# Kernel optimization log

Measured on AMD Instinct MI355X. Metric: run time of the kernel, lower is better.

## Reference

```python
import jax, jax.numpy as jnp
import numpy as np

NUM_KNOTS = 10
DEGREE = 3
NUM_BASIS = NUM_KNOTS + DEGREE - 1  # 12
IN_FEATURES = 512
OUT_FEATURES = 512


def _interval_bounds():
    # t = linspace(0,1,num_knots); segment i covers [t[max(0,i-deg+1)], t[min(i+1,K-1)])
    t = np.linspace(0.0, 1.0, NUM_KNOTS, dtype=np.float32)
    idx = np.arange(NUM_BASIS)
    lower = t[np.maximum(0, idx - (DEGREE - 1))]
    upper = t[np.minimum(idx + 1, NUM_KNOTS - 1)]
    return jnp.asarray(lower), jnp.asarray(upper)


def setup_inputs() -> dict:
    key = jax.random.key(0)
    kx, kc = jax.random.split(key)
    x = jax.random.uniform(kx, (8, 2048, IN_FEATURES), dtype=jnp.float32)
    # coeffs for spline (i=out, j=in): torch indexes splines[i*in_features+j]
    coeffs = jax.random.normal(kc, (OUT_FEATURES, IN_FEATURES, NUM_BASIS), dtype=jnp.float32)
    return {"x": x, "coeffs": coeffs}


def reference(x, coeffs):
    lower, upper = _interval_bounds()  # [NUM_BASIS] each
    # piecewise-constant basis masks: [b, s, in, NUM_BASIS]
    xe = x[..., None]
    basis = ((xe >= lower) & (xe < upper)).astype(x.dtype)
    # out[b,s,i] = sum_j sum_k basis[b,s,j,k] * coeffs[i,j,k]
    return jnp.einsum("bsjk,ijk->bsi", basis, coeffs)
```

## Files before the change

kernel.cpp:

```cpp
#include <hip/hip_runtime.h>

#define MTOT 16384
#define NFEAT 512
#define KTOT 4608

typedef float f32x4 __attribute__((ext_vector_type(4)));
typedef short s16x8 __attribute__((ext_vector_type(8)));

__device__ __forceinline__ int div9(int c) { return (c * 7282) >> 16; }

#define GLDS(GP, LP) __builtin_amdgcn_global_load_lds( \
    (const __attribute__((address_space(1))) void*)(GP), \
    (__attribute__((address_space(3))) void*)(LP), 16, 0, 0)

__device__ __forceinline__ s16x8 decode_mask(unsigned msk) {
  unsigned e0 = (msk & 15u) * 0x00204081u & 0x01010101u;
  unsigned e1 = (msk >> 4)  * 0x00204081u & 0x01010101u;
  unsigned d0 = __builtin_amdgcn_perm(e0, e0, 0x0C010C00u) * 0x3F80u;
  unsigned d1 = __builtin_amdgcn_perm(e0, e0, 0x0C030C02u) * 0x3F80u;
  unsigned d2 = __builtin_amdgcn_perm(e1, e1, 0x0C010C00u) * 0x3F80u;
  unsigned d3 = __builtin_amdgcn_perm(e1, e1, 0x0C030C02u) * 0x3F80u;
  union { unsigned d[4]; s16x8 v; } u;
  u.d[0] = d0; u.d[1] = d1; u.d[2] = d2; u.d[3] = d3;
  return u.v;
}

__global__ __launch_bounds__(256) void prep(const float* __restrict__ x,
                                            const float* __restrict__ coeffs,
                                            unsigned char* __restrict__ codeT,
                                            unsigned short* __restrict__ Bmat) {
  __shared__ unsigned char segt[64][68];
  const int bx = blockIdx.x;
  const int tid = threadIdx.x;
  if (bx < 2048) {
    const int i = bx >> 2, q = bx & 3;
    const float* cb = coeffs + (size_t)i * 6144;
#pragma unroll
    for (int p = 0; p < 5; ++p) {
      int kl = p * 256 + tid;
      if (kl < 1152) {
        int k = q * 1152 + kl;
        int j = div9(k), s = k - j * 9;
        float v = cb[j * 12 + s] + cb[j * 12 + s + 1] + cb[j * 12 + s + 2];
        unsigned u = __float_as_uint(v);
        unsigned rn = (u + 0x7FFFu + ((u >> 16) & 1u)) >> 16;
        Bmat[(size_t)i * KTOT + k] = (unsigned short)rn;
      }
    }
  } else {
    const int bb = bx - 2048;
    const int mt = bb >> 3;
    const int jt = bb & 7;
    const int m0 = mt * 64;
    const float4* x4 = (const float4*)x;
    const float T1 = (float)(1.0/9.0), T2 = (float)(2.0/9.0), T3 = (float)(3.0/9.0),
                T4 = (float)(4.0/9.0), T5 = (float)(5.0/9.0), T6 = (float)(6.0/9.0),
                T7 = (float)(7.0/9.0), T8 = (float)(8.0/9.0);
#pragma unroll
    for (int it = 0; it < 4; ++it) {
      int f = it * 256 + tid;
      int m = f >> 4, jq = f & 15;
      float4 v = x4[(size_t)(m0 + m) * 128 + jt * 16 + jq];
      uchar4 sv;
      { float xv = v.x; sv.x = (unsigned char)((xv>=T1)+(xv>=T2)+(xv>=T3)+(xv>=T4)+(xv>=T5)+(xv>=T6)+(xv>=T7)+(xv>=T8)); }
      { float xv = v.y; sv.y = (unsigned char)((xv>=T1)+(xv>=T2)+(xv>=T3)+(xv>=T4)+(xv>=T5)+(xv>=T6)+(xv>=T7)+(xv>=T8)); }
      { float xv = v.z; sv.z = (unsigned char)((xv>=T1)+(xv>=T2)+(xv>=T3)+(xv>=T4)+(xv>=T5)+(xv>=T6)+(xv>=T7)+(xv>=T8)); }
      { float xv = v.w; sv.w = (unsigned char)((xv>=T1)+(xv>=T2)+(xv>=T3)+(xv>=T4)+(xv>=T5)+(xv>=T6)+(xv>=T7)+(xv>=T8)); }
      *(uchar4*)&segt[m][jq * 4] = sv;
    }
    __syncthreads();
#pragma unroll
    for (int p = 0; p < 5; ++p) {
      int u = p * 256 + tid;
      if (u < 1152) {
        int gl = u >> 4, mq = u & 15;
        int c0 = jt * 576 + gl * 8;
        int j0 = div9(c0), j1 = div9(c0 + 7);
        int j0l = j0 - jt * 64, j1l = j1 - jt * 64;
        uchar4 ob;
        unsigned char* pb = (unsigned char*)&ob;
#pragma unroll
        for (int c = 0; c < 4; ++c) {
          int m = mq * 4 + c;
          int s0 = segt[m][j0l];
          int pos0 = j0 * 9 + s0 - c0;
          unsigned code = (pos0 >= 0 && pos0 < 8) ? (1u << pos0) : 0u;
          if (j1 != j0) {
            int s1 = segt[m][j1l];
            int pos1 = j1 * 9 + s1 - c0;
            if (pos1 < 8) code |= (1u << pos1);
          }
          pb[c] = (unsigned char)code;
        }
        *(uchar4*)(codeT + (size_t)(jt * 72 + gl) * MTOT + m0 + mq * 4) = ob;
      }
    }
  }
}

__global__ __launch_bounds__(256, 4) void kan_gemm(const unsigned char* __restrict__ codeT,
                                                   const unsigned short* __restrict__ Bmat,
                                                   float* __restrict__ out) {
  __shared__ __align__(16) short Blds[2][8 * 512];
  const int tid = threadIdx.x;
  const int lane = tid & 63;
  const int wid = tid >> 6;
  const int lm = lane & 15;
  const int lq = lane >> 4;
  const int bx = blockIdx.x;
  const int nt = bx & 7;
  const int mt = bx >> 3;
  const int m0 = mt * 128, n0 = nt * 64;

  const unsigned short* gB = Bmat + (size_t)(n0 + wid * 16 + lm) * KTOT + lq * 8;
  const unsigned char* gC0 = codeT + (size_t)lq * MTOT + m0 + wid * 32 + lm;
  const unsigned char* gC1 = codeT + (size_t)(4 + lq) * MTOT + m0 + wid * 32 + lm;

  f32x4 acc[2][4] = {};
  s16x8 afA[4], afB[4];
  unsigned char cr[4];

#define LOAD_CR() do { \
    cr[0] = gC0[0]; cr[1] = gC1[0]; cr[2] = gC0[16]; cr[3] = gC1[16]; \
    gC0 += (size_t)8 * MTOT; gC1 += (size_t)8 * MTOT; } while (0)

#define ISSUE_B(buf) do { \
    short* base = &Blds[buf][0] + wid * 1024; \
    GLDS(gB,      base);        \
    GLDS(gB + 32, base + 512);  \
    gB += 64; } while (0)

#define COMPUTE(AF, buf) do { \
    _Pragma("unroll") \
    for (int ks = 0; ks < 2; ++ks) { \
      s16x8 bf[4]; \
      _Pragma("unroll") \
      for (int ns = 0; ns < 4; ++ns) \
        bf[ns] = *(const s16x8*)&Blds[buf][(ns * 2 + ks) * 512 + lane * 8]; \
      _Pragma("unroll") \
      for (int ms = 0; ms < 2; ++ms) \
        _Pragma("unroll") \
        for (int ns = 0; ns < 4; ++ns) \
          acc[ms][ns] = __builtin_amdgcn_mfma_f32_16x16x32_bf16(AF[ms * 2 + ks], bf[ns], acc[ms][ns], 0, 0, 0); \
    } } while (0)

  LOAD_CR();
  ISSUE_B(0);
#pragma unroll
  for (int f = 0; f < 4; ++f) afA[f] = decode_mask(cr[f]);
  LOAD_CR();
  __syncthreads();

#pragma unroll 1
  for (int kt = 0; kt < 72; kt += 2) {
    ISSUE_B(1);
#pragma unroll
    for (int f = 0; f < 4; ++f) afB[f] = decode_mask(cr[f]);
    if (kt < 70) LOAD_CR();
    COMPUTE(afA, 0);
    __syncthreads();
    if (kt < 70) {
      ISSUE_B(0);
#pragma unroll
      for (int f = 0; f < 4; ++f) afA[f] = decode_mask(cr[f]);
      LOAD_CR();
    }
    COMPUTE(afB, 1);
    __syncthreads();
  }

#pragma unroll
  for (int ms = 0; ms < 2; ++ms) {
#pragma unroll
    for (int ns = 0; ns < 4; ++ns) {
      int tok = m0 + wid * 32 + ms * 16 + lq * 4;
      int col = n0 + ns * 16 + lm;
      float* op = out + (size_t)tok * NFEAT + col;
#pragma unroll
      for (int rg = 0; rg < 4; ++rg) op[(size_t)rg * NFEAT] = acc[ms][ns][rg];
    }
  }
}

extern "C" void kernel_launch(void* const* d_in, const int* in_sizes, int n_in,
                              void* d_out, int out_size, void* d_ws, size_t ws_size,
                              hipStream_t stream) {
  const float* x = (const float*)d_in[0];
  const float* coeffs = (const float*)d_in[1];
  float* out = (float*)d_out;
  unsigned char* codeT = (unsigned char*)d_ws;
  unsigned short* Bmat = (unsigned short*)((char*)d_ws + (size_t)576 * MTOT);

  prep<<<dim3(4096), dim3(256), 0, stream>>>(x, coeffs, codeT, Bmat);
  kan_gemm<<<dim3(1024), dim3(256), 0, stream>>>(codeT, Bmat, out);
}
```

Measured before the change: 173.3 us.

## Switch GEMM to 32x32x16 MFMA with 256-row tiles and inline mask decode

Replaces the 16x16x32 bf16 MFMA tiling with 32x32x16 MFMA, doubling the M tile per block to 256 rows and halving the grid to 512 blocks. Each wave now computes a 64x64 output tile, so each B fragment loaded from LDS is reused across more rows, and the LDS layout and global-to-LDS loads are reorganised to match. Mask decoding moves inside the compute loop instead of being precomputed one stage ahead. Occupancy hint drops from 4 to 2 blocks per CU, with larger accumulators per thread. With only 512 blocks, CU utilisation may suffer on a 256-CU part.

```diff
diff --git a/kernel.cpp b/kernel.cpp
--- a/kernel.cpp
+++ b/kernel.cpp
@@ -4,7 +4,7 @@
 #define NFEAT 512
 #define KTOT 4608
 
-typedef float f32x4 __attribute__((ext_vector_type(4)));
+typedef float f32x16 __attribute__((ext_vector_type(16)));
 typedef short s16x8 __attribute__((ext_vector_type(8)));
 
 __device__ __forceinline__ int div9(int c) { return (c * 7282) >> 16; }
@@ -98,86 +98,86 @@
   }
 }
 
-__global__ __launch_bounds__(256, 4) void kan_gemm(const unsigned char* __restrict__ codeT,
+__global__ __launch_bounds__(256, 2) void kan_gemm(const unsigned char* __restrict__ codeT,
                                                    const unsigned short* __restrict__ Bmat,
                                                    float* __restrict__ out) {
   __shared__ __align__(16) short Blds[2][8 * 512];
   const int tid = threadIdx.x;
   const int lane = tid & 63;
   const int wid = tid >> 6;
-  const int lm = lane & 15;
-  const int lq = lane >> 4;
+  const int l5 = lane & 31;
+  const int lh = lane >> 5;
   const int bx = blockIdx.x;
   const int nt = bx & 7;
   const int mt = bx >> 3;
-  const int m0 = mt * 128, n0 = nt * 64;
+  const int m0 = mt * 256, n0 = nt * 64;
 
-  const unsigned short* gB = Bmat + (size_t)(n0 + wid * 16 + lm) * KTOT + lq * 8;
-  const unsigned char* gC0 = codeT + (size_t)lq * MTOT + m0 + wid * 32 + lm;
-  const unsigned char* gC1 = codeT + (size_t)(4 + lq) * MTOT + m0 + wid * 32 + lm;
+  const int s0 = 2 * wid, s1 = 2 * wid + 1;
+  const unsigned short* gB0 = Bmat + (size_t)(n0 + (s0 >> 2) * 32 + l5) * KTOT + (s0 & 3) * 16 + lh * 8;
+  const unsigned short* gB1 = Bmat + (size_t)(n0 + (s1 >> 2) * 32 + l5) * KTOT + (s1 & 3) * 16 + lh * 8;
+  const unsigned char* gCk0 = codeT + (size_t)(0 * 2 + lh) * MTOT + m0 + wid * 64 + l5;
+  const unsigned char* gCk1 = codeT + (size_t)(1 * 2 + lh) * MTOT + m0 + wid * 64 + l5;
+  const unsigned char* gCk2 = codeT + (size_t)(2 * 2 + lh) * MTOT + m0 + wid * 64 + l5;
+  const unsigned char* gCk3 = codeT + (size_t)(3 * 2 + lh) * MTOT + m0 + wid * 64 + l5;
 
-  f32x4 acc[2][4] = {};
-  s16x8 afA[4], afB[4];
-  unsigned char cr[4];
+  f32x16 acc[2][2] = {};
+  unsigned char crA[8], crB[8];
 
-#define LOAD_CR() do { \
-    cr[0] = gC0[0]; cr[1] = gC1[0]; cr[2] = gC0[16]; cr[3] = gC1[16]; \
-    gC0 += (size_t)8 * MTOT; gC1 += (size_t)8 * MTOT; } while (0)
+#define LOAD_CR(CR) do { \
+    CR[0] = gCk0[0];  CR[4] = gCk0[32]; \
+    CR[1] = gCk1[0];  CR[5] = gCk1[32]; \
+    CR[2] = gCk2[0];  CR[6] = gCk2[32]; \
+    CR[3] = gCk3[0];  CR[7] = gCk3[32]; \
+    gCk0 += (size_t)8 * MTOT; gCk1 += (size_t)8 * MTOT; \
+    gCk2 += (size_t)8 * MTOT; gCk3 += (size_t)8 * MTOT; } while (0)
 
 #define ISSUE_B(buf) do { \
-    short* base = &Blds[buf][0] + wid * 1024; \
-    GLDS(gB,      base);        \
-    GLDS(gB + 32, base + 512);  \
-    gB += 64; } while (0)
+    GLDS(gB0, &Blds[buf][0] + s0 * 512); \
+    GLDS(gB1, &Blds[buf][0] + s1 * 512); \
+    gB0 += 64; gB1 += 64; } while (0)
 
-#define COMPUTE(AF, buf) do { \
+#define COMPUTE(CR, buf) do { \
     _Pragma("unroll") \
-    for (int ks = 0; ks < 2; ++ks) { \
-      s16x8 bf[4]; \
+    for (int ks = 0; ks < 4; ++ks) { \
+      s16x8 b0 = *(const s16x8*)&Blds[buf][(0 * 4 + ks) * 512 + lane * 8]; \
+      s16x8 b1 = *(const s16x8*)&Blds[buf][(1 * 4 + ks) * 512 + lane * 8]; \
       _Pragma("unroll") \
-      for (int ns = 0; ns < 4; ++ns) \
-        bf[ns] = *(const s16x8*)&Blds[buf][(ns * 2 + ks) * 512 + lane * 8]; \
-      _Pragma("unroll") \
-      for (int ms = 0; ms < 2; ++ms) \
-        _Pragma("unroll") \
-        for (int ns = 0; ns < 4; ++ns) \
-          acc[ms][ns] = __builtin_amdgcn_mfma_f32_16x16x32_bf16(AF[ms * 2 + ks], bf[ns], acc[ms][ns], 0, 0, 0); \
+      for (int ms = 0; ms < 2; ++ms) { \
+        s16x8 a = decode_mask(CR[ms * 4 + ks]); \
+        acc[ms][0] = __builtin_amdgcn_mfma_f32_32x32x16_bf16(a, b0, acc[ms][0], 0, 0, 0); \
+        acc[ms][1] = __builtin_amdgcn_mfma_f32_32x32x16_bf16(a, b1, acc[ms][1], 0, 0, 0); \
+      } \
     } } while (0)
 
-  LOAD_CR();
+  LOAD_CR(crA);
   ISSUE_B(0);
-#pragma unroll
-  for (int f = 0; f < 4; ++f) afA[f] = decode_mask(cr[f]);
-  LOAD_CR();
+  LOAD_CR(crB);
   __syncthreads();
 
 #pragma unroll 1
   for (int kt = 0; kt < 72; kt += 2) {
     ISSUE_B(1);
-#pragma unroll
-    for (int f = 0; f < 4; ++f) afB[f] = decode_mask(cr[f]);
-    if (kt < 70) LOAD_CR();
-    COMPUTE(afA, 0);
+    COMPUTE(crA, 0);
+    if (kt < 70) LOAD_CR(crA);
     __syncthreads();
-    if (kt < 70) {
-      ISSUE_B(0);
-#pragma unroll
-      for (int f = 0; f < 4; ++f) afA[f] = decode_mask(cr[f]);
-      LOAD_CR();
-    }
-    COMPUTE(afB, 1);
+    if (kt < 70) ISSUE_B(0);
+    COMPUTE(crB, 1);
+    if (kt < 70) LOAD_CR(crB);
     __syncthreads();
   }
 
 #pragma unroll
   for (int ms = 0; ms < 2; ++ms) {
 #pragma unroll
-    for (int ns = 0; ns < 4; ++ns) {
-      int tok = m0 + wid * 32 + ms * 16 + lq * 4;
-      int col = n0 + ns * 16 + lm;
-      float* op = out + (size_t)tok * NFEAT + col;
+    for (int ns = 0; ns < 2; ++ns) {
+      int rowbase = m0 + wid * 64 + ms * 32 + 4 * lh;
+      int col = n0 + ns * 32 + l5;
+      float* op = out + (size_t)rowbase * NFEAT + col;
 #pragma unroll
-      for (int rg = 0; rg < 4; ++rg) op[(size_t)rg * NFEAT] = acc[ms][ns][rg];
+      for (int rg = 0; rg < 16; ++rg) {
+        int row_off = (rg & 3) + 8 * (rg >> 2);
+        op[(size_t)row_off * NFEAT] = acc[ms][ns][rg];
+      }
     }
   }
 }
@@ -192,5 +192,5 @@
   unsigned short* Bmat = (unsigned short*)((char*)d_ws + (size_t)576 * MTOT);
 
   prep<<<dim3(4096), dim3(256), 0, stream>>>(x, coeffs, codeT, Bmat);
-  kan_gemm<<<dim3(1024), dim3(256), 0, stream>>>(codeT, Bmat, out);
+  kan_gemm<<<dim3(512), dim3(256), 0, stream>>>(codeT, Bmat, out);
 }
```

After: 173.3 us. No clear change (+0.0%).
